# Kernel optimization log

Measured on AMD Instinct MI355X. Metric: run time of the kernel, lower is better.

Reference implementation:

```python
import jax, jax.numpy as jnp
import numpy as np


def setup_inputs() -> dict:
    key = jax.random.key(0)
    ks = jax.random.split(key, 6)
    B, Cin, H, W = 8, 512, 128, 128
    Ck, Cv, K = 256, 256, 64
    s = lambda fan: fan ** -0.5
    return {
        "x": jax.random.normal(ks[0], (B, Cin, H, W), jnp.float32),
        "context": jax.random.normal(ks[1], (B, Cv, K), jnp.float32),
        "Wq": jax.random.normal(ks[2], (Ck, Cin), jnp.float32) * s(Cin),
        "Wk": jax.random.normal(ks[3], (Ck, Cv), jnp.float32) * s(Cv),
        "Wv": jax.random.normal(ks[4], (Cv, Cv), jnp.float32) * s(Cv),
        "Wp": jax.random.normal(ks[5], (Cin, Cv), jnp.float32) * s(Cv),
    }


def reference(x, context, Wq, Wk, Wv, Wp):
    B, Cin, H, W = x.shape
    Ck = Wq.shape[0]
    scale = Ck ** -0.5
    xf = x.reshape(B, Cin, H * W)                      # [B, Cin, N]
    q = jnp.einsum("kc,bcn->bnk", Wq, xf)             # [B, N, Ck]
    k = jnp.einsum("kc,bcm->bkm", Wk, context)        # [B, Ck, K]
    v = jnp.einsum("vc,bcm->bmv", Wv, context)        # [B, K, Cv]
    sim = jnp.einsum("bnk,bkm->bnm", q, k) * scale    # [B, N, K]
    attn = jax.nn.softmax(sim, axis=-1)
    out = jnp.einsum("bnm,bmv->bnv", attn, v)         # [B, N, Cv]
    out = jnp.einsum("cv,bnv->bcn", Wp, out)          # [B, Cin, N]
    return out.reshape(B, Cin, H, W)
```

## Files before the change

### kernel.cpp

```cpp
#include <hip/hip_runtime.h>
#include <stdint.h>

#define B_    8
#define CIN   512
#define NPIX  16384
#define CK    256
#define KCTX  64
#define CV    256

typedef _Float16 f16;
typedef _Float16 f16x4 __attribute__((ext_vector_type(4)));
typedef _Float16 f16x8 __attribute__((ext_vector_type(8)));
typedef float    f32x4 __attribute__((ext_vector_type(4)));

#define LOG2E 1.44269504f

#define WQK_OFF 0
#define WPV_OFF 524288

__global__ __launch_bounds__(1024) void prep(const float* __restrict__ ctx,
                                             const float* __restrict__ Wk,
                                             const float* __restrict__ Wv,
                                             const float* __restrict__ Wq,
                                             const float* __restrict__ Wp,
                                             char* __restrict__ ws) {
    __shared__ char lds[65536];
    char* ctx_t = lds;
    char* kv_s  = lds + 32768;

    const int p = blockIdx.x;
    const int b = blockIdx.y;
    const int path = p >> 1, h = p & 1;
    const int t = threadIdx.x;
    const int w = t >> 6, l = t & 63, g = l >> 4, ln = l & 15;

    {
        const int m4 = (t & 15) * 4, c4 = (t >> 4) * 4;
        const float* cp = ctx + (size_t)b * (CV * KCTX) + (size_t)c4 * KCTX + m4;
        f32x4 xr[4];
        #pragma unroll
        for (int i = 0; i < 4; ++i) xr[i] = *(const f32x4*)(cp + (size_t)i * KCTX);
        #pragma unroll
        for (int j = 0; j < 4; ++j) {
            f16x4 v4; v4[0] = (f16)xr[0][j]; v4[1] = (f16)xr[1][j]; v4[2] = (f16)xr[2][j]; v4[3] = (f16)xr[3][j];
            int m = m4 + j;
            *(f16x4*)(ctx_t + m * 512 + 16 * (((c4 >> 3) & 31) ^ (m & 7)) + 2 * (c4 & 7)) = v4;
        }
    }
    __syncthreads();

    {
        const float* W = path ? Wv : Wk;
        const int rbase = 64 * (w >> 2);
        const int mm = 16 * (w & 3) + ln;
        f32x4 acc[4] = {};
        for (int ks = 0; ks < 8; ++ks) {
            f16x8 bf = *(const f16x8*)(ctx_t + mm * 512 + 16 * ((4 * ks + g) ^ (mm & 7)));
            #pragma unroll
            for (int mi = 0; mi < 4; ++mi) {
                int row = rbase + 16 * mi + ln;
                const float* wp0 = W + (size_t)row * CV + 32 * ks + 8 * g;
                f32x4 lo = *(const f32x4*)wp0, hi = *(const f32x4*)(wp0 + 4);
                f16x8 af;
                #pragma unroll
                for (int j = 0; j < 4; ++j) { af[j] = (f16)lo[j]; af[4 + j] = (f16)hi[j]; }
                acc[mi] = __builtin_amdgcn_mfma_f32_16x16x32_f16(af, bf, acc[mi], 0, 0, 0);
            }
        }
        #pragma unroll
        for (int mi = 0; mi < 4; ++mi)
            #pragma unroll
            for (int r = 0; r < 4; ++r) {
                int row = rbase + 16 * mi + 4 * g + r;
                *(f16*)(kv_s + mm * 512 + 16 * ((((row >> 3) & 31)) ^ (mm & 7)) + 2 * (row & 7)) = (f16)acc[mi][r];
            }
    }
    __syncthreads();

    if (path == 0) {
        f32x4 acc2[4] = {};
        const int cA = 256 * h + 16 * w + ln;
        const float* qcol = Wq + cA;
        for (int ks = 0; ks < 8; ++ks) {
            f16x8 af;
            #pragma unroll
            for (int j = 0; j < 8; ++j)
                af[j] = (f16)qcol[(size_t)(32 * ks + 8 * g + j) * CIN];
            #pragma unroll
            for (int ni = 0; ni < 4; ++ni) {
                int m2 = 16 * ni + ln;
                f16x8 bf = *(const f16x8*)(kv_s + m2 * 512 + 16 * ((4 * ks + g) ^ (m2 & 7)));
                acc2[ni] = __builtin_amdgcn_mfma_f32_16x16x32_f16(af, bf, acc2[ni], 0, 0, 0);
            }
        }
        char* dst = ws + WQK_OFF + b * 65536;
        #pragma unroll
        for (int ni = 0; ni < 4; ++ni)
            #pragma unroll
            for (int r = 0; r < 4; ++r) {
                int c = 256 * h + 16 * w + 4 * g + r;
                int s  = c >> 6, kk = (c >> 5) & 1, gk = (c >> 3) & 3, j = c & 7;
                int byte = ((((s * 4 + ni) * 2 + kk) * 4 + gk) * 16 + ln) * 16 + 2 * j;
                *(f16*)(dst + byte) = (f16)(acc2[ni][r] * 0.0625f);
            }
    } else {
        f32x4 acc2[4] = {};
        const int cA = 256 * h + 16 * w + ln;
        for (int ks = 0; ks < 8; ++ks) {
            const float* pp = Wp + (size_t)cA * CV + 32 * ks + 8 * g;
            f32x4 lo = *(const f32x4*)pp, hi = *(const f32x4*)(pp + 4);
            f16x8 af;
            #pragma unroll
            for (int j = 0; j < 4; ++j) { af[j] = (f16)lo[j]; af[4 + j] = (f16)hi[j]; }
            #pragma unroll
            for (int ni = 0; ni < 4; ++ni) {
                int m2 = 16 * ni + ln;
                f16x8 bf = *(const f16x8*)(kv_s + m2 * 512 + 16 * ((4 * ks + g) ^ (m2 & 7)));
                acc2[ni] = __builtin_amdgcn_mfma_f32_16x16x32_f16(af, bf, acc2[ni], 0, 0, 0);
            }
        }
        char* dst = ws + WPV_OFF + b * 65536;
        #pragma unroll
        for (int ni = 0; ni < 4; ++ni) {
            const int kkm = ni >> 1;
            const int gm  = ln >> 2;
            const int jm  = 4 * (ni & 1) + (ln & 3);
            #pragma unroll
            for (int r = 0; r < 4; ++r) {
                int c = 256 * h + 16 * w + 4 * g + r;
                int ct = c >> 4, lnc = c & 15;
                int byte = (((ct * 2 + kkm) * 4 + gm) * 16 + lnc) * 16 + 2 * jm;
                *(f16*)(dst + byte) = (f16)acc2[ni][r];
            }
        }
    }
}

__global__ __launch_bounds__(256, 4) void fused(const float* __restrict__ x,
                                                const char* __restrict__ ws,
                                                float* __restrict__ out) {
    __shared__ char lds[32768];
    const int b = blockIdx.y;
    const int t = threadIdx.x;
    const int w = t >> 6, l = t & 63, g = l >> 4, ln = l & 15;
    const int nb = blockIdx.x * 128 + 32 * w;
    char* wl = lds + w * 8192;

    const char* wqk = ws + WQK_OFF + b * 65536;
    const char* wpv = ws + WPV_OFF + b * 65536;
    const float* xb = x + (size_t)b * CIN * NPIX + nb;

    const int n4 = 4 * (l & 7);
    const int cg0 = (l >> 3);

    f32x4 xr[2][4];

#define STAGE_LOAD(S)                                                          \
    {                                                                          \
        _Pragma("unroll")                                                      \
        for (int u = 0; u < 2; ++u) {                                          \
            const float* xp = xb + (size_t)(64 * (S) + 4 * (cg0 + 8 * u)) * NPIX + n4; \
            _Pragma("unroll")                                                  \
            for (int i = 0; i < 4; ++i)                                        \
                xr[u][i] = *(const f32x4*)(xp + (size_t)i * NPIX);             \
        }                                                                      \
    }

#define STAGE_WRITE(BUF)                                                       \
    {                                                                          \
        _Pragma("unroll")                                                      \
        for (int u = 0; u < 2; ++u) {                                          \
            int cg = cg0 + 8 * u;                                              \
            _Pragma("unroll")                                                  \
            for (int j = 0; j < 4; ++j) {                                      \
                f16x4 v4;                                                      \
                v4[0] = (f16)xr[u][0][j]; v4[1] = (f16)xr[u][1][j];            \
                v4[2] = (f16)xr[u][2][j]; v4[3] = (f16)xr[u][3][j];            \
                int nl = n4 + j;                                               \
                int fn = (nl ^ (nl >> 3)) & 7;                                 \
                *(f16x4*)((BUF) + nl * 128 + 16 * ((cg >> 1) ^ fn) + 8 * (cg & 1)) = v4; \
            }                                                                  \
        }                                                                      \
    }

    f32x4 accs[2][4] = {};
    STAGE_LOAD(0);
    STAGE_WRITE(wl);
    #pragma unroll
    for (int s = 0; s < 8; ++s) {
        const char* cur = wl + (s & 1) * 4096;
        if (s < 7) STAGE_LOAD(s + 1);
        #pragma unroll
        for (int kk = 0; kk < 2; ++kk) {
            f16x8 bf[2];
            #pragma unroll
            for (int nt = 0; nt < 2; ++nt) {
                int nl = 16 * nt + ln;
                int fn = (nl ^ (nl >> 3)) & 7;
                bf[nt] = *(const f16x8*)(cur + nl * 128 + 16 * ((4 * kk + g) ^ fn));
            }
            #pragma unroll
            for (int mi = 0; mi < 4; ++mi) {
                f16x8 af = *(const f16x8*)(wqk + ((((s * 4 + mi) * 2 + kk) * 4 + g) * 16 + ln) * 16);
                accs[0][mi] = __builtin_amdgcn_mfma_f32_16x16x32_f16(af, bf[0], accs[0][mi], 0, 0, 0);
                accs[1][mi] = __builtin_amdgcn_mfma_f32_16x16x32_f16(af, bf[1], accs[1][mi], 0, 0, 0);
            }
        }
        if (s < 7) STAGE_WRITE(wl + ((s + 1) & 1) * 4096);
    }

    f16x8 afr[2][2];
    #pragma unroll
    for (int nt = 0; nt < 2; ++nt) {
        float mx = accs[nt][0][0];
        #pragma unroll
        for (int mi = 0; mi < 4; ++mi)
            #pragma unroll
            for (int r = 0; r < 4; ++r) mx = fmaxf(mx, accs[nt][mi][r]);
        mx = fmaxf(mx, __shfl_xor(mx, 16, 64));
        mx = fmaxf(mx, __shfl_xor(mx, 32, 64));
        float pv[4][4];
        float sum = 0.f;
        #pragma unroll
        for (int mi = 0; mi < 4; ++mi)
            #pragma unroll
            for (int r = 0; r < 4; ++r) {
                float pe = __builtin_amdgcn_exp2f((accs[nt][mi][r] - mx) * LOG2E);
                pv[mi][r] = pe; sum += pe;
            }
        sum += __shfl_xor(sum, 16, 64);
        sum += __shfl_xor(sum, 32, 64);
        float inv = 1.f / sum;
        #pragma unroll
        for (int kk = 0; kk < 2; ++kk)
            #pragma unroll
            for (int j = 0; j < 8; ++j)
                afr[nt][kk][j] = (f16)(pv[2 * kk + (j >> 2)][j & 3] * inv);
    }

    float* ob = out + (size_t)b * CIN * NPIX + nb + 4 * g;
    #pragma unroll 4
    for (int ct = 0; ct < 32; ++ct) {
        int c = 16 * ct + ln;
        f32x4 acc0 = {}, acc1 = {};
        #pragma unroll
        for (int kk = 0; kk < 2; ++kk) {
            f16x8 bfp = *(const f16x8*)(wpv + (((ct * 2 + kk) * 4 + g) * 16 + ln) * 16);
            acc0 = __builtin_amdgcn_mfma_f32_16x16x32_f16(afr[0][kk], bfp, acc0, 0, 0, 0);
            acc1 = __builtin_amdgcn_mfma_f32_16x16x32_f16(afr[1][kk], bfp, acc1, 0, 0, 0);
        }
        *(f32x4*)(ob + (size_t)c * NPIX)      = acc0;
        *(f32x4*)(ob + (size_t)c * NPIX + 16) = acc1;
    }
}

extern "C" void kernel_launch(void* const* d_in, const int* in_sizes, int n_in,
                              void* d_out, int out_size, void* d_ws, size_t ws_size,
                              hipStream_t stream) {
    (void)in_sizes; (void)n_in; (void)out_size; (void)ws_size;
    const float* x   = (const float*)d_in[0];
    const float* ctx = (const float*)d_in[1];
    const float* Wq  = (const float*)d_in[2];
    const float* Wk  = (const float*)d_in[3];
    const float* Wv  = (const float*)d_in[4];
    const float* Wp  = (const float*)d_in[5];
    float* out = (float*)d_out;
    char* ws = (char*)d_ws;

    prep<<<dim3(4, B_), 1024, 0, stream>>>(ctx, Wk, Wv, Wq, Wp, ws);
    fused<<<dim3(NPIX / 128, B_), 256, 0, stream>>>(x, ws, out);
}
```

Before: 178.2 us.

## Split fused attention kernel into separate sim/softmax and output-projection kernels

Breaks the single fused kernel into two. The first computes q·k, applies softmax and writes fp16 attention weights to workspace. The second reads those weights and runs the output projection with a smaller per-wave tile and higher occupancy. The aim is to separate the read-heavy phase from the write-heavy phase so each kernel can run at its own occupancy. The cost is an extra round trip of 32 MB of attention weights through global memory and one more kernel launch. An unused gl_lds16 helper is also added.

Measured after the change: 193.6 us. 8.7% more time.

```diff
diff --git a/kernel.cpp b/kernel.cpp
--- a/kernel.cpp
+++ b/kernel.cpp
@@ -15,8 +15,15 @@
 
 #define LOG2E 1.44269504f
 
-#define WQK_OFF 0
-#define WPV_OFF 524288
+#define WQK_OFF  0
+#define WPV_OFF  524288
+#define ATTN_OFF 1048576
+
+__device__ __forceinline__ void gl_lds16(const void* g, void* l) {
+    __builtin_amdgcn_global_load_lds(
+        (const __attribute__((address_space(1))) uint32_t*)g,
+        (__attribute__((address_space(3))) uint32_t*)l, 16, 0, 0);
+}
 
 __global__ __launch_bounds__(1024) void prep(const float* __restrict__ ctx,
                                              const float* __restrict__ Wk,
@@ -136,9 +143,9 @@
     }
 }
 
-__global__ __launch_bounds__(256, 4) void fused(const float* __restrict__ x,
-                                                const char* __restrict__ ws,
-                                                float* __restrict__ out) {
+__global__ __launch_bounds__(256, 4) void simk(const float* __restrict__ x,
+                                               const char* __restrict__ ws,
+                                               char* __restrict__ attn) {
     __shared__ char lds[32768];
     const int b = blockIdx.y;
     const int t = threadIdx.x;
@@ -147,7 +154,6 @@
     char* wl = lds + w * 8192;
 
     const char* wqk = ws + WQK_OFF + b * 65536;
-    const char* wpv = ws + WPV_OFF + b * 65536;
     const float* xb = x + (size_t)b * CIN * NPIX + nb;
 
     const int n4 = 4 * (l & 7);
@@ -209,7 +215,6 @@
         if (s < 7) STAGE_WRITE(wl + ((s + 1) & 1) * 4096);
     }
 
-    f16x8 afr[2][2];
     #pragma unroll
     for (int nt = 0; nt < 2; ++nt) {
         float mx = accs[nt][0][0];
@@ -231,26 +236,45 @@
         sum += __shfl_xor(sum, 16, 64);
         sum += __shfl_xor(sum, 32, 64);
         float inv = 1.f / sum;
-        #pragma unroll
-        for (int kk = 0; kk < 2; ++kk)
+        const int n = nb + 16 * nt + ln;
+        char* ap = attn + ((size_t)b * NPIX + n) * 128 + 16 * g;
+        #pragma unroll
+        for (int kk = 0; kk < 2; ++kk) {
+            f16x8 afr;
             #pragma unroll
             for (int j = 0; j < 8; ++j)
-                afr[nt][kk][j] = (f16)(pv[2 * kk + (j >> 2)][j & 3] * inv);
-    }
+                afr[j] = (f16)(pv[2 * kk + (j >> 2)][j & 3] * inv);
+            *(f16x8*)(ap + kk * 64) = afr;
+        }
+    }
+}
+
+__global__ __launch_bounds__(256, 8) void outk(const char* __restrict__ attn,
+                                               const char* __restrict__ ws,
+                                               float* __restrict__ out) {
+    const int b = blockIdx.y;
+    const int t = threadIdx.x;
+    const int w = t >> 6, l = t & 63, g = l >> 4, ln = l & 15;
+    const int nb = blockIdx.x * 64 + 16 * w;
+
+    const char* wpv = ws + WPV_OFF + b * 65536;
+    const char* ap = attn + ((size_t)b * NPIX + nb + ln) * 128 + 16 * g;
+
+    f16x8 afr[2];
+    afr[0] = *(const f16x8*)(ap);
+    afr[1] = *(const f16x8*)(ap + 64);
 
     float* ob = out + (size_t)b * CIN * NPIX + nb + 4 * g;
     #pragma unroll 4
     for (int ct = 0; ct < 32; ++ct) {
         int c = 16 * ct + ln;
-        f32x4 acc0 = {}, acc1 = {};
+        f32x4 acc = {};
         #pragma unroll
         for (int kk = 0; kk < 2; ++kk) {
             f16x8 bfp = *(const f16x8*)(wpv + (((ct * 2 + kk) * 4 + g) * 16 + ln) * 16);
-            acc0 = __builtin_amdgcn_mfma_f32_16x16x32_f16(afr[0][kk], bfp, acc0, 0, 0, 0);
-            acc1 = __builtin_amdgcn_mfma_f32_16x16x32_f16(afr[1][kk], bfp, acc1, 0, 0, 0);
-        }
-        *(f32x4*)(ob + (size_t)c * NPIX)      = acc0;
-        *(f32x4*)(ob + (size_t)c * NPIX + 16) = acc1;
+            acc = __builtin_amdgcn_mfma_f32_16x16x32_f16(afr[kk], bfp, acc, 0, 0, 0);
+        }
+        *(f32x4*)(ob + (size_t)c * NPIX) = acc;
     }
 }
 
@@ -268,5 +292,6 @@
     char* ws = (char*)d_ws;
 
     prep<<<dim3(4, B_), 1024, 0, stream>>>(ctx, Wk, Wv, Wq, Wp, ws);
-    fused<<<dim3(NPIX / 128, B_), 256, 0, stream>>>(x, ws, out);
-}
+    simk<<<dim3(NPIX / 128, B_), 256, 0, stream>>>(x, ws, ws + ATTN_OFF);
+    outk<<<dim3(NPIX / 64, B_), 256, 0, stream>>>(ws + ATTN_OFF, ws, out);
+}
```
